# Performance work log

Hardware: AMD Instinct MI355X
Metric: run time of the kernel (lower is better)

The kernel has to match this reference:

```python
import jax, jax.numpy as jnp
import numpy as np

IGNORE_INDEX = 255
LOG_CLAMP = 100.0  # torch BCE clamps log at -100, so -log(x) <= 100


def _neg_log(x, cond):
    # BCE(x, 1) = -log(x), with the torch clamp log(x) >= -100.
    x_safe = jnp.where(cond, jnp.maximum(x, 1e-38), 1.0)
    return jnp.where(cond, jnp.minimum(-jnp.log(x_safe), LOG_CLAMP), 0.0)


def setup_inputs() -> dict:
    key = jax.random.key(0)
    k1, k2 = jax.random.split(key)
    B, C, H, W, D = 1, 20, 256, 256, 32
    pred = jax.random.normal(k1, (B, C, H, W, D), dtype=jnp.float32)
    target = jax.random.randint(k2, (B, H, W, D), 0, C, dtype=jnp.int64)
    return {"pred": pred, "target": target}


def reference(pred, target):
    C = pred.shape[1]
    p = jax.nn.softmax(pred, axis=1)                      # [B,C,H,W,D]
    mask = (target != IGNORE_INDEX)                        # [B,H,W,D]

    # Flatten voxels: [N, C] probs, [N] labels, [N] mask.
    p_flat = jnp.moveaxis(p, 1, -1).reshape(-1, C)
    t_flat = target.reshape(-1)
    m_flat = mask.reshape(-1).astype(p.dtype)
    t_safe = jnp.where(mask.reshape(-1), t_flat, 0).astype(jnp.int32)

    # Per-class reductions in one pass (replaces the per-class python loop):
    # nominator[c] = sum_{masked, t==c} p_c ; ct_count[c] = |{masked, t==c}|
    p_at_t = jnp.take_along_axis(p_flat, t_safe[:, None], axis=1)[:, 0] * m_flat
    nominator = jax.ops.segment_sum(p_at_t, t_safe, num_segments=C)
    ct_count = jax.ops.segment_sum(m_flat, t_safe, num_segments=C)
    sum_p = jnp.einsum('nc,n->c', p_flat, m_flat)          # sum of p_c over masked
    n_masked = jnp.sum(m_flat)

    neg_count = n_masked - ct_count                        # sum(1 - ct)
    spec_num = n_masked - sum_p - ct_count + nominator     # sum((1-p)(1-ct))

    valid = ct_count > 0
    prec = nominator / jnp.maximum(sum_p, 1e-38)
    rec = nominator / jnp.maximum(ct_count, 1.0)
    spec = spec_num / jnp.maximum(neg_count, 1.0)

    loss_c = (_neg_log(prec, valid & (sum_p > 0))
              + _neg_log(rec, valid)
              + _neg_log(spec, valid & (neg_count > 0)))
    count = jnp.sum(valid.astype(p.dtype))
    return jnp.sum(loss_c) / count
```

## Files before the change

kernel.cpp:

```cpp
#include <hip/hip_runtime.h>
#include <math.h>

#define NCLS 20
#define IGNORE_IDX 255
#define LOG2E 1.4426950408889634f
#define NTHR 256
#define VOXPT 4
#define NSLOT 32

__device__ __forceinline__ float wave_reduce(float v) {
#pragma unroll
  for (int off = 32; off > 0; off >>= 1) v += __shfl_xor(v, off, 64);
  return v;
}

__device__ __forceinline__ float neg_log_clamped(float x, bool cond) {
  if (!cond) return 0.0f;
  float xs = fmaxf(x, 1e-38f);
  return fminf(-logf(xs), 100.0f);
}

__global__ __launch_bounds__(NTHR, 4) void pass1(const float* __restrict__ pred,
                                                 const int* __restrict__ target,
                                                 float* __restrict__ ws, int N) {
  __shared__ float s_acc[3 * NCLS][32];
  const int tid = threadIdx.x;
  const int sl = tid & 31;

  {
    float* p = &s_acc[0][0];
    for (int i = tid; i < 3 * NCLS * 32; i += NTHR) p[i] = 0.0f;
  }
  __syncthreads();

  float accp[NCLS];
#pragma unroll
  for (int c = 0; c < NCLS; ++c) accp[c] = 0.0f;

  const int base = blockIdx.x * (NTHR * VOXPT);
#pragma unroll 1
  for (int it = 0; it < VOXPT; ++it) {
    const int n = base + it * NTHR + tid;
    if (n < N) {
      const int t = target[n];

      float Z = 0.0f, pt = 0.0f;
#pragma unroll
      for (int c = 0; c < NCLS; ++c) {
        const float x = pred[(size_t)c * N + n];
        const float e = __builtin_amdgcn_exp2f(fminf(x, 80.0f) * LOG2E);
        Z += e;
        pt = (c == t) ? e : pt;
      }
      const bool msk = (t != IGNORE_IDX);
      const float w = msk ? __builtin_amdgcn_rcpf(Z) : 0.0f;
      if (msk) {
        atomicAdd(&s_acc[NCLS + t][sl], pt * w);
        atomicAdd(&s_acc[2 * NCLS + t][sl], 1.0f);
      }

#pragma unroll
      for (int c = 0; c < NCLS; ++c) {
        const float x = pred[(size_t)c * N + n];
        const float e = __builtin_amdgcn_exp2f(fminf(x, 80.0f) * LOG2E);
        accp[c] += e * w;
      }
    }
  }

#pragma unroll
  for (int c = 0; c < NCLS; ++c) atomicAdd(&s_acc[c][sl], accp[c]);
  __syncthreads();

  if (tid < 3 * NCLS) {
    const float* row = s_acc[tid];
    float v = 0.0f;
#pragma unroll
    for (int i = 0; i < 32; ++i) v += row[(i + tid) & 31];
    atomicAdd(&ws[(size_t)(blockIdx.x & (NSLOT - 1)) * 64 + tid], v);
  }
}

__global__ __launch_bounds__(64) void pass2(const float* __restrict__ ws,
                                            float* __restrict__ out) {
  __shared__ float s[64];
  const int lane = threadIdx.x;
  float a = 0.0f;
#pragma unroll
  for (int r = 0; r < NSLOT; ++r) a += ws[r * 64 + lane];

  const float n_masked =
      wave_reduce((lane >= 2 * NCLS && lane < 3 * NCLS) ? a : 0.0f);

  s[lane] = a;
  __syncthreads();

  float loss = 0.0f, validf = 0.0f;
  if (lane < NCLS) {
    const float sump = s[lane];
    const float nom = s[NCLS + lane];
    const float cnt = s[2 * NCLS + lane];
    const bool valid = cnt > 0.0f;
    const float prec = nom / fmaxf(sump, 1e-38f);
    const float rec = nom / fmaxf(cnt, 1.0f);
    const float negc = n_masked - cnt;
    const float specn = n_masked - sump - cnt + nom;
    const float spec = specn / fmaxf(negc, 1.0f);
    loss = neg_log_clamped(prec, valid && (sump > 0.0f)) +
           neg_log_clamped(rec, valid) +
           neg_log_clamped(spec, valid && (negc > 0.0f));
    validf = valid ? 1.0f : 0.0f;
  }
  loss = wave_reduce(loss);
  validf = wave_reduce(validf);
  if (lane == 0) out[0] = loss / validf;
}

extern "C" void kernel_launch(void* const* d_in, const int* in_sizes, int n_in,
                              void* d_out, int out_size, void* d_ws, size_t ws_size,
                              hipStream_t stream) {
  const float* pred = (const float*)d_in[0];
  const int* target = (const int*)d_in[1];
  const int N = in_sizes[1];
  const int per_blk = NTHR * VOXPT;
  const int nblk = (N + per_blk - 1) / per_blk;

  hipMemsetAsync(d_ws, 0, NSLOT * 64 * sizeof(float), stream);
  pass1<<<nblk, NTHR, 0, stream>>>(pred, target, (float*)d_ws, N);
  pass2<<<1, 64, 0, stream>>>((const float*)d_ws, (float*)d_out);
}
```

Measured before the change: 285.6 us.

## Double-buffer pred tiles into LDS via async global_load_lds in persistent blocks

Switches pass1 to a fixed grid of 512 persistent blocks, each looping over 256-voxel chunks. Each chunk's 20 class rows are prefetched into a double-buffered LDS tile with global_load_lds, and the next chunk's load overlaps the current chunk's compute. The second exp pass now reads from LDS instead of reloading from global memory. It also replaces the per-thread register accumulators with per-voxel LDS atomics for sum_p, which adds LDS atomic traffic and two barriers per chunk.

Measured after the change: 425.8 us. 1.49x slower.

```diff
diff --git a/kernel.cpp b/kernel.cpp
--- a/kernel.cpp
+++ b/kernel.cpp
@@ -5,7 +5,8 @@
 #define IGNORE_IDX 255
 #define LOG2E 1.4426950408889634f
 #define NTHR 256
-#define VOXPT 4
+#define HALF 256
+#define NBLK 512
 #define NSLOT 32
 
 __device__ __forceinline__ float wave_reduce(float v) {
@@ -20,11 +21,21 @@
   return fminf(-logf(xs), 100.0f);
 }
 
-__global__ __launch_bounds__(NTHR, 4) void pass1(const float* __restrict__ pred,
-                                                 const int* __restrict__ target,
-                                                 float* __restrict__ ws, int N) {
+__device__ __forceinline__ void gload_lds16(const float* g, float* l) {
+  __builtin_amdgcn_global_load_lds(
+      (const __attribute__((address_space(1))) void*)g,
+      (__attribute__((address_space(3))) void*)l, 16, 0, 0);
+}
+
+__global__ __launch_bounds__(NTHR) void pass1(const float* __restrict__ pred,
+                                              const int* __restrict__ target,
+                                              float* __restrict__ ws, int N,
+                                              int HPB) {
+  __shared__ float s_x[2][NCLS * HALF];
   __shared__ float s_acc[3 * NCLS][32];
   const int tid = threadIdx.x;
+  const int wid = tid >> 6;
+  const int lane = tid & 63;
   const int sl = tid & 31;
 
   {
@@ -33,44 +44,75 @@
   }
   __syncthreads();
 
-  float accp[NCLS];
+  const long long g0 = (long long)blockIdx.x * HPB;
+
+  int t_next;
+  {
+    long long nn = g0 * HALF + tid;
+    if (nn > N - 1) nn = N - 1;
+    t_next = target[nn];
+    const int e0 = (int)((g0 * HALF + lane * 4 > (long long)N - 4)
+                             ? (long long)N - 4
+                             : g0 * HALF + lane * 4);
 #pragma unroll
-  for (int c = 0; c < NCLS; ++c) accp[c] = 0.0f;
+    for (int i = 0; i < 5; ++i) {
+      const int c = wid + 4 * i;
+      gload_lds16(pred + (size_t)c * N + e0, &s_x[0][c * HALF]);
+    }
+  }
 
-  const int base = blockIdx.x * (NTHR * VOXPT);
-#pragma unroll 1
-  for (int it = 0; it < VOXPT; ++it) {
-    const int n = base + it * NTHR + tid;
-    if (n < N) {
-      const int t = target[n];
+  for (int it = 0; it < HPB; ++it) {
+    const int hb = it & 1;
+    const int t_cur = t_next;
+    const long long g = g0 + it;
+    const bool more = (it + 1 < HPB);
 
+    if (more) {
+      long long nn = (g + 1) * HALF + tid;
+      if (nn > N - 1) nn = N - 1;
+      t_next = target[nn];
+      const int e0 = (int)(((g + 1) * HALF + lane * 4 > (long long)N - 4)
+                               ? (long long)N - 4
+                               : (g + 1) * HALF + lane * 4);
+#pragma unroll
+      for (int i = 0; i < 5; ++i) {
+        const int c = wid + 4 * i;
+        gload_lds16(pred + (size_t)c * N + e0, &s_x[hb ^ 1][c * HALF]);
+      }
+      asm volatile("s_waitcnt vmcnt(6)" ::: "memory");
+    } else {
+      asm volatile("s_waitcnt vmcnt(0)" ::: "memory");
+    }
+    __builtin_amdgcn_sched_barrier(0);
+    __syncthreads();
+
+    {
+      const float* sx = &s_x[hb][0];
+      const long long n = g * HALF + tid;
+      const bool in = (n < N);
       float Z = 0.0f, pt = 0.0f;
 #pragma unroll
       for (int c = 0; c < NCLS; ++c) {
-        const float x = pred[(size_t)c * N + n];
-        const float e = __builtin_amdgcn_exp2f(fminf(x, 80.0f) * LOG2E);
+        const float e =
+            __builtin_amdgcn_exp2f(fminf(sx[c * HALF + tid], 80.0f) * LOG2E);
         Z += e;
-        pt = (c == t) ? e : pt;
+        pt = (c == t_cur) ? e : pt;
       }
-      const bool msk = (t != IGNORE_IDX);
+      const bool msk = in && (t_cur != IGNORE_IDX);
       const float w = msk ? __builtin_amdgcn_rcpf(Z) : 0.0f;
       if (msk) {
-        atomicAdd(&s_acc[NCLS + t][sl], pt * w);
-        atomicAdd(&s_acc[2 * NCLS + t][sl], 1.0f);
+        atomicAdd(&s_acc[NCLS + t_cur][sl], pt * w);
+        atomicAdd(&s_acc[2 * NCLS + t_cur][sl], 1.0f);
       }
-
 #pragma unroll
       for (int c = 0; c < NCLS; ++c) {
-        const float x = pred[(size_t)c * N + n];
-        const float e = __builtin_amdgcn_exp2f(fminf(x, 80.0f) * LOG2E);
-        accp[c] += e * w;
+        const float e =
+            __builtin_amdgcn_exp2f(fminf(sx[c * HALF + tid], 80.0f) * LOG2E);
+        atomicAdd(&s_acc[c][sl], e * w);
       }
     }
+    __syncthreads();
   }
-
-#pragma unroll
-  for (int c = 0; c < NCLS; ++c) atomicAdd(&s_acc[c][sl], accp[c]);
-  __syncthreads();
 
   if (tid < 3 * NCLS) {
     const float* row = s_acc[tid];
@@ -122,10 +164,10 @@
   const float* pred = (const float*)d_in[0];
   const int* target = (const int*)d_in[1];
   const int N = in_sizes[1];
-  const int per_blk = NTHR * VOXPT;
-  const int nblk = (N + per_blk - 1) / per_blk;
+  const int NH = (N + HALF - 1) / HALF;
+  const int HPB = (NH + NBLK - 1) / NBLK;
 
   hipMemsetAsync(d_ws, 0, NSLOT * 64 * sizeof(float), stream);
-  pass1<<<nblk, NTHR, 0, stream>>>(pred, target, (float*)d_ws, N);
+  pass1<<<NBLK, NTHR, 0, stream>>>(pred, target, (float*)d_ws, N, HPB);
   pass2<<<1, 64, 0, stream>>>((const float*)d_ws, (float*)d_out);
 }
```
